# Kernel optimization log

Hardware: AMD Instinct MI355X
Metric: run time of the kernel (lower is better)

The kernel has to match this reference:

```python
import jax, jax.numpy as jnp
import numpy as np

JACCARD_THRESH = 0.5
NEGPOS_RATIO = 3
V0, V1 = 0.1, 0.2  # SSD encoding variances


def setup_inputs() -> dict:
    key = jax.random.key(0)
    k1, k2, k3, k4, k5, k6, k7 = jax.random.split(key, 7)
    B, P, C, O = 128, 8732, 21, 16
    loc_data = jax.random.normal(k1, (B, P, 4), dtype=jnp.float32)
    conf_data = jax.random.normal(k2, (B, P, C), dtype=jnp.float32)
    # default boxes in center form (cx, cy, w, h), all in [0,1]
    cxcy = jax.random.uniform(k3, (P, 2), minval=0.05, maxval=0.95)
    wh = jax.random.uniform(k4, (P, 2), minval=0.05, maxval=0.6)
    dbox_list = jnp.concatenate([cxcy, wh], axis=1).astype(jnp.float32)
    # ground-truth boxes in corner form with guaranteed positive extent
    tl = jax.random.uniform(k5, (B, O, 2), minval=0.0, maxval=0.6)
    sz = jax.random.uniform(k6, (B, O, 2), minval=0.05, maxval=0.35)
    labels = jax.random.randint(k7, (B, O, 1), 0, C - 1).astype(jnp.float32)
    targets = jnp.concatenate([tl, tl + sz, labels], axis=2)
    return {"loc_data": loc_data, "conf_data": conf_data,
            "dbox_list": dbox_list, "targets": targets}


def _match_one(truths, labels, dbox):
    """SSD match for one image. truths:[O,4] corner, labels:[O], dbox:[P,4] center."""
    pf = jnp.concatenate([dbox[:, :2] - dbox[:, 2:] * 0.5,
                          dbox[:, :2] + dbox[:, 2:] * 0.5], axis=1)  # point form [P,4]
    lt = jnp.maximum(truths[:, None, :2], pf[None, :, :2])
    rb = jnp.minimum(truths[:, None, 2:], pf[None, :, 2:])
    whi = jnp.clip(rb - lt, 0.0)
    inter = whi[..., 0] * whi[..., 1]                                # [O,P]
    area_t = (truths[:, 2] - truths[:, 0]) * (truths[:, 3] - truths[:, 1])
    area_p = dbox[:, 2] * dbox[:, 3]
    ov = inter / (area_t[:, None] + area_p[None, :] - inter)         # jaccard [O,P]
    best_prior_idx = jnp.argmax(ov, axis=1)                          # [O]
    bto = jnp.max(ov, axis=0)                                        # [P]
    bti = jnp.argmax(ov, axis=0)                                     # [P]
    bto = bto.at[best_prior_idx].set(2.0)
    O = truths.shape[0]
    bti = jax.lax.fori_loop(0, O, lambda j, b: b.at[best_prior_idx[j]].set(j), bti)
    matched = truths[bti]                                            # [P,4]
    conf = labels[bti].astype(jnp.int32) + 1
    conf = jnp.where(bto < JACCARD_THRESH, 0, conf)
    g_cxcy = ((matched[:, :2] + matched[:, 2:]) * 0.5 - dbox[:, :2]) / (V0 * dbox[:, 2:])
    g_wh = jnp.log((matched[:, 2:] - matched[:, :2]) / dbox[:, 2:]) / V1
    return jnp.concatenate([g_cxcy, g_wh], axis=1), conf


def reference(loc_data, conf_data, dbox_list, targets):
    B, P, C = conf_data.shape
    loc_t, conf_t = jax.vmap(_match_one, in_axes=(0, 0, None))(
        targets[..., :4], targets[..., 4], dbox_list)
    pos = conf_t > 0                                                  # [B,P]
    # smooth L1 (beta=1), summed over positives
    ad = jnp.abs(loc_data - loc_t)
    sl1 = jnp.where(ad < 1.0, 0.5 * ad * ad, ad - 0.5)
    loss_l = jnp.sum(jnp.where(pos[..., None], sl1, 0.0))
    # per-prior cross entropy
    logp = jax.nn.log_softmax(conf_data, axis=-1)
    ce = -jnp.take_along_axis(logp, conf_t[..., None], axis=-1)[..., 0]  # [B,P]
    # hard negative mining via double argsort (rank in descending order)
    ce_neg = jnp.where(pos, 0.0, ce)
    loss_idx = jnp.argsort(-ce_neg, axis=1)
    idx_rank = jnp.argsort(loss_idx, axis=1)
    num_pos = jnp.sum(pos, axis=1, keepdims=True)
    num_neg = jnp.minimum(num_pos * NEGPOS_RATIO, P)
    neg = idx_rank < num_neg
    sel = pos | neg
    loss_c = jnp.sum(jnp.where(sel, ce, 0.0))
    N = jnp.sum(num_pos).astype(loc_data.dtype)
    return jnp.stack([loss_l / N, loss_c / N])
```

## Files before the change

### kernel.cpp

```cpp
#include <hip/hip_runtime.h>
#include <cstddef>

#define Bn 128
#define Pn 8732
#define Cn 21
#define On 16
#define MAGIC 0x13579BDFu

__device__ __forceinline__ void argmax_combine(float& v, int& p, float v2, int p2) {
  if (v2 > v || (v2 == v && p2 < p)) { v = v2; p = p2; }
}

__global__ __launch_bounds__(256) void stream_kernel(
    const float* __restrict__ conf, const float* __restrict__ dbox,
    const float* __restrict__ targets,
    float* __restrict__ ce0, unsigned char* __restrict__ pack,
    unsigned long long* __restrict__ keys) {
  const int wb = threadIdx.x >> 6, lane = threadIdx.x & 63;
  const int wave_g = blockIdx.x * 4 + wb;
  const int b = wave_g & 127;
  const int cg = wave_g >> 7;

  __shared__ float4 s_row4[4][336];
  __shared__ float s_tt[4][On * 5];
  __shared__ float s_ar[4][On];

  #pragma unroll
  for (int i = lane; i < On * 5; i += 64)
    s_tt[wb][i] = targets[(size_t)b * On * 5 + i];
  if (lane < On) {
    float x1 = targets[(size_t)b * On * 5 + lane * 5 + 0];
    float y1 = targets[(size_t)b * On * 5 + lane * 5 + 1];
    float x2 = targets[(size_t)b * On * 5 + lane * 5 + 2];
    float y2 = targets[(size_t)b * On * 5 + lane * 5 + 3];
    s_ar[wb][lane] = (x2 - x1) * (y2 - y1);
  }

  float bestv[On]; int bestp[On];
  #pragma unroll
  for (int j = 0; j < On; j++) { bestv[j] = -1.0f; bestp[j] = 0x7fffffff; }

  #pragma unroll
  for (int i = 0; i < 3; i++) {
    const int ci = cg + 64 * i;
    if (ci >= 137) break;
    const int p0 = ci * 64;
    const int rows = min(64, Pn - p0);
    const int n4 = rows * Cn / 4;

    const float4* src = (const float4*)(conf + ((size_t)b * Pn + p0) * Cn);
    float4 v0, v1, v2, v3, v4, v5;
    if (lane < n4)        v0 = src[lane];
    if (lane + 64 < n4)   v1 = src[lane + 64];
    if (lane + 128 < n4)  v2 = src[lane + 128];
    if (lane + 192 < n4)  v3 = src[lane + 192];
    if (lane + 256 < n4)  v4 = src[lane + 256];
    if (lane + 320 < n4)  v5 = src[lane + 320];
    if (lane < n4)        s_row4[wb][lane] = v0;
    if (lane + 64 < n4)   s_row4[wb][lane + 64] = v1;
    if (lane + 128 < n4)  s_row4[wb][lane + 128] = v2;
    if (lane + 192 < n4)  s_row4[wb][lane + 192] = v3;
    if (lane + 256 < n4)  s_row4[wb][lane + 256] = v4;
    if (lane + 320 < n4)  s_row4[wb][lane + 320] = v5;

    if (lane < rows) {
      const int p = p0 + lane;
      const float* x = (const float*)s_row4[wb] + lane * Cn;
      float m = x[0];
      #pragma unroll
      for (int q = 1; q < Cn; q++) m = fmaxf(m, x[q]);
      float s = 0.0f;
      #pragma unroll
      for (int q = 0; q < Cn; q++) s += __expf(x[q] - m);
      float lse = m + __logf(s);
      ce0[(size_t)b * Pn + p] = lse - x[0];

      float4 d = ((const float4*)dbox)[p];
      float px1 = d.x - d.z * 0.5f, py1 = d.y - d.w * 0.5f;
      float px2 = d.x + d.z * 0.5f, py2 = d.y + d.w * 0.5f;
      float ap = d.z * d.w;
      float mv = -1.0f; int mj = 0;
      #pragma unroll
      for (int j = 0; j < On; j++) {
        float lx = fmaxf(s_tt[wb][j*5+0], px1);
        float ly = fmaxf(s_tt[wb][j*5+1], py1);
        float rx = fminf(s_tt[wb][j*5+2], px2);
        float ry = fminf(s_tt[wb][j*5+3], py2);
        float w = fmaxf(rx - lx, 0.0f), h = fmaxf(ry - ly, 0.0f);
        float inter = w * h;
        float ov = __fdividef(inter, s_ar[wb][j] + ap - inter);
        if (ov > bestv[j]) { bestv[j] = ov; bestp[j] = p; }
        if (ov > mv) { mv = ov; mj = j; }
      }
      pack[(size_t)b * Pn + p] =
          (unsigned char)(mj | ((mv >= 0.5f) ? 16 : 0));
    }
  }

  #pragma unroll
  for (int j = 0; j < On; j++) {
    float v = bestv[j]; int p = bestp[j];
    #pragma unroll
    for (int off = 32; off; off >>= 1) {
      float v2 = __shfl_down(v, off);
      int p2 = __shfl_down(p, off);
      argmax_combine(v, p, v2, p2);
    }
    if (lane == 0) {
      unsigned long long key;
      if (v < 0.0f) key = 0xC000000000000000ull;
      else key = (((unsigned long long)(__float_as_uint(v) | 0xC0000000u)) << 32)
               | (unsigned long long)(0xFFFFFFFFu - (unsigned)p);
      atomicMax(&keys[b * On + j], key);
    }
  }
}

__global__ __launch_bounds__(1024) void reduce_kernel(
    const float* __restrict__ loc, const float* __restrict__ conf,
    const float* __restrict__ dbox, const float* __restrict__ targets,
    const float* __restrict__ ce0, const unsigned char* __restrict__ pack,
    const unsigned long long* __restrict__ keys,
    unsigned int* __restrict__ res, float* __restrict__ out) {
  const int b = blockIdx.x;
  const int tid = threadIdx.x;
  const int wave = tid >> 6, lane = tid & 63;

  __shared__ float s_t[On * 5];
  __shared__ int s_bp[On];
  __shared__ unsigned hist[256 * 16];
  __shared__ unsigned s_col[256];
  __shared__ unsigned s_cand[64];
  __shared__ float s_redf[2][16];
  __shared__ int s_redi[16];
  __shared__ unsigned s_prefix;
  __shared__ int s_kk;
  __shared__ int s_cnt;
  __shared__ int s_cc;
  __shared__ int s_np;

  if (tid < On * 5) s_t[tid] = targets[(size_t)b * On * 5 + tid];
  if (tid < On)
    s_bp[tid] = (int)(0xFFFFFFFFu - (unsigned)(keys[b * On + tid] & 0xFFFFFFFFull));
  __syncthreads();

  float ce_r[9];
  float my_loc = 0.0f, my_cep = 0.0f; int my_np = 0;
  #pragma unroll
  for (int sI = 0; sI < 9; sI++) {
    ce_r[sI] = 0.0f;
    const int p = tid + 1024 * sI;
    if (p < Pn) {
      unsigned char pk = pack[(size_t)b * Pn + p];
      float c0 = ce0[(size_t)b * Pn + p];
      int pos = pk >> 4;
      int bt = pk & 15;
      #pragma unroll
      for (int j = 0; j < On; j++)
        if (s_bp[j] == p) { bt = j; pos = 1; }
      ce_r[sI] = pos ? 0.0f : c0;
      if (pos) {
        my_np++;
        const float* t = &s_t[bt * 5];
        int c = (int)t[4] + 1;
        const float* row = conf + ((size_t)b * Pn + p) * Cn;
        my_cep += c0 + row[0] - row[c];
        float4 d = ((const float4*)dbox)[p];
        float mx1 = t[0], my1 = t[1], mx2 = t[2], my2 = t[3];
        float g0 = ((mx1 + mx2) * 0.5f - d.x) / (0.1f * d.z);
        float g1 = ((my1 + my2) * 0.5f - d.y) / (0.1f * d.w);
        float g2 = logf((mx2 - mx1) / d.z) / 0.2f;
        float g3 = logf((my2 - my1) / d.w) / 0.2f;
        float4 ld = ((const float4*)loc)[(size_t)b * Pn + p];
        float g[4] = {g0, g1, g2, g3};
        float l[4] = {ld.x, ld.y, ld.z, ld.w};
        #pragma unroll
        for (int q = 0; q < 4; q++) {
          float ad = fabsf(l[q] - g[q]);
          my_loc += (ad < 1.0f) ? 0.5f * ad * ad : ad - 0.5f;
        }
      }
    }
  }

  {
    int np = my_np;
    #pragma unroll
    for (int off = 32; off; off >>= 1) np += __shfl_down(np, off);
    if (lane == 0) s_redi[wave] = np;
  }
  __syncthreads();
  if (tid == 0) {
    int np = 0;
    #pragma unroll
    for (int w = 0; w < 16; w++) np += s_redi[w];
    s_np = np;
  }
  __syncthreads();

  const int k = min(s_np * 3, Pn);
  unsigned prefix = 0, maskb = 0;
  int kk = k;
  int cntc = Pn;
  for (int shift = 24; shift >= 0; shift -= 8) {
    if (cntc <= 64) break;
    ((uint4*)hist)[tid] = make_uint4(0u, 0u, 0u, 0u);
    __syncthreads();
    #pragma unroll
    for (int sI = 0; sI < 9; sI++) {
      const int p = tid + 1024 * sI;
      if (p < Pn) {
        unsigned u = __float_as_uint(ce_r[sI]);
        if ((u & maskb) == prefix)
          atomicAdd(&hist[(((u >> shift) & 255u) << 4) + (unsigned)wave], 1u);
      }
    }
    __syncthreads();
    if (tid < 256) {
      unsigned c = 0;
      #pragma unroll
      for (int w = 0; w < 16; w++) c += hist[(tid << 4) + w];
      s_col[tid] = c;
    }
    __syncthreads();
    if (tid < 64) {
      unsigned c0 = s_col[4 * tid + 0], c1 = s_col[4 * tid + 1];
      unsigned c2 = s_col[4 * tid + 2], c3 = s_col[4 * tid + 3];
      unsigned t0 = c0 + c1 + c2 + c3;
      unsigned S = t0;
      #pragma unroll
      for (int off = 1; off < 64; off <<= 1) {
        unsigned o = __shfl_down(S, off);
        if (tid + off < 64) S += o;
      }
      unsigned Snext = S - t0;
      unsigned s3 = Snext + c3;
      unsigned s2 = s3 + c2;
      unsigned s1 = s2 + c1;
      unsigned s0 = s1 + c0;
      unsigned kk_u = (unsigned)kk;
      int chosen = -1; unsigned snx = 0, cc = 0;
      if (s3 >= kk_u && Snext < kk_u)      { chosen = 3; snx = Snext; cc = c3; }
      else if (s2 >= kk_u && s3 < kk_u)    { chosen = 2; snx = s3;    cc = c2; }
      else if (s1 >= kk_u && s2 < kk_u)    { chosen = 1; snx = s2;    cc = c1; }
      else if (s0 >= kk_u && s1 < kk_u)    { chosen = 0; snx = s1;    cc = c0; }
      if (chosen >= 0) {
        s_prefix = prefix | ((unsigned)(4 * tid + chosen) << shift);
        s_kk = (int)(kk_u - snx);
        s_cnt = (int)cc;
      }
    }
    __syncthreads();
    prefix = s_prefix; kk = s_kk; cntc = s_cnt;
    maskb |= 255u << shift;
  }
  if (maskb != 0xFFFFFFFFu) {
    if (tid == 0) s_cc = 0;
    __syncthreads();
    #pragma unroll
    for (int sI = 0; sI < 9; sI++) {
      const int p = tid + 1024 * sI;
      if (p < Pn) {
        unsigned u = __float_as_uint(ce_r[sI]);
        if ((u & maskb) == prefix) {
          int ix = atomicAdd(&s_cc, 1);
          s_cand[ix] = u;
        }
      }
    }
    __syncthreads();
    if (tid < 64) {
      int c = s_cc;
      if (tid < c) {
        unsigned v = s_cand[tid];
        int g = 0, e = 0;
        for (int i = 0; i < c; i++) {
          unsigned w = s_cand[i];
          g += (w > v); e += (w == v);
        }
        if (g < kk && kk <= g + e) s_prefix = v;
      }
    }
    __syncthreads();
    prefix = s_prefix;
  }
  float T = __uint_as_float(prefix);

  float sum_gt = 0.0f; int cnt_gt = 0;
  #pragma unroll
  for (int sI = 0; sI < 9; sI++) {
    const int p = tid + 1024 * sI;
    if (p < Pn) {
      float x = ce_r[sI];
      if (x > T) { sum_gt += x; cnt_gt++; }
    }
  }
  #pragma unroll
  for (int off = 32; off; off >>= 1) {
    sum_gt += __shfl_down(sum_gt, off);
    cnt_gt += __shfl_down(cnt_gt, off);
    my_loc += __shfl_down(my_loc, off);
    my_cep += __shfl_down(my_cep, off);
  }
  if (lane == 0) {
    s_redf[0][wave] = my_loc; s_redf[1][wave] = sum_gt + my_cep; s_redi[wave] = cnt_gt;
  }
  __syncthreads();
  if (tid == 0) {
    float ll = 0.0f, lc = 0.0f; int cg = 0;
    #pragma unroll
    for (int w = 0; w < 16; w++) {
      ll += s_redf[0][w]; lc += s_redf[1][w]; cg += s_redi[w];
    }
    lc += (k > 0) ? (float)(k - cg) * T : 0.0f;
    atomicExch(&res[b * 4 + 0], __float_as_uint(ll));
    atomicExch(&res[b * 4 + 1], __float_as_uint(lc));
    atomicExch(&res[b * 4 + 2], (unsigned)s_np);
    __threadfence();
    atomicExch(&res[b * 4 + 3], MAGIC);
  }

  if (b == 0 && tid < 64) {
    float ll = 0.0f, lc = 0.0f; int np = 0;
    #pragma unroll
    for (int h = 0; h < 2; h++) {
      const int i = tid + 64 * h;
      while (atomicAdd(&res[i * 4 + 3], 0u) != MAGIC) { __builtin_amdgcn_s_sleep(8); }
      ll += __uint_as_float(atomicAdd(&res[i * 4 + 0], 0u));
      lc += __uint_as_float(atomicAdd(&res[i * 4 + 1], 0u));
      np += (int)atomicAdd(&res[i * 4 + 2], 0u);
    }
    #pragma unroll
    for (int off = 32; off; off >>= 1) {
      ll += __shfl_down(ll, off);
      lc += __shfl_down(lc, off);
      np += __shfl_down(np, off);
    }
    if (tid == 0) {
      float fN = (float)np;
      out[0] = ll / fN;
      out[1] = lc / fN;
    }
  }
}

extern "C" void kernel_launch(void* const* d_in, const int* in_sizes, int n_in,
                              void* d_out, int out_size, void* d_ws, size_t ws_size,
                              hipStream_t stream) {
  const float* loc_data  = (const float*)d_in[0];
  const float* conf_data = (const float*)d_in[1];
  const float* dbox      = (const float*)d_in[2];
  const float* targets   = (const float*)d_in[3];
  float* out = (float*)d_out;

  char* ws = (char*)d_ws;
  float* ce0 = (float*)ws;
  unsigned char* pack = (unsigned char*)(ws + (size_t)Bn * Pn * 4);
  unsigned long long* keys =
      (unsigned long long*)(ws + (size_t)Bn * Pn * 5);
  unsigned int* res = (unsigned int*)(ws + (size_t)Bn * Pn * 5 + Bn * On * 8);

  stream_kernel<<<2048, 256, 0, stream>>>(conf_data, dbox, targets, ce0, pack, keys);
  reduce_kernel<<<Bn, 1024, 0, stream>>>(loc_data, conf_data, dbox, targets,
                                         ce0, pack, keys, res, out);
}
```

Measured before the change: 205.2 us.

## Halve stream grid and handle forced-match priors via bitmask and dedicated wave

The stream kernel now launches half as many blocks, and each wave walks up to five 64-prior chunks instead of three. In the reduce kernel, the 16-way compare per prior is replaced by a shared bitmask lookup of the forced best-prior indices. Those forced priors have their CE and localization loss computed separately by wave 0 with a full log-sum-exp, presumably because ce0 may not hold the right value for them. It also uses the fast __logf intrinsic and bounds the candidate buffer writes, trading a little accuracy and some added serial work in wave 0 for less per-prior overhead.

```diff
diff --git a/kernel.cpp b/kernel.cpp
--- a/kernel.cpp
+++ b/kernel.cpp
@@ -9,6 +9,20 @@
 
 __device__ __forceinline__ void argmax_combine(float& v, int& p, float v2, int p2) {
   if (v2 > v || (v2 == v && p2 < p)) { v = v2; p = p2; }
+}
+
+__device__ __forceinline__ float sl1_enc(float4 lv, float4 d,
+                                         float t0, float t1, float t2, float t3) {
+  float g0 = ((t0 + t2) * 0.5f - d.x) / (0.1f * d.z);
+  float g1 = ((t1 + t3) * 0.5f - d.y) / (0.1f * d.w);
+  float g2 = __logf((t2 - t0) / d.z) / 0.2f;
+  float g3 = __logf((t3 - t1) / d.w) / 0.2f;
+  float r = 0.f, a;
+  a = fabsf(lv.x - g0); r += (a < 1.f) ? 0.5f * a * a : a - 0.5f;
+  a = fabsf(lv.y - g1); r += (a < 1.f) ? 0.5f * a * a : a - 0.5f;
+  a = fabsf(lv.z - g2); r += (a < 1.f) ? 0.5f * a * a : a - 0.5f;
+  a = fabsf(lv.w - g3); r += (a < 1.f) ? 0.5f * a * a : a - 0.5f;
+  return r;
 }
 
 __global__ __launch_bounds__(256) void stream_kernel(
@@ -25,7 +39,6 @@
   __shared__ float s_tt[4][On * 5];
   __shared__ float s_ar[4][On];
 
-  #pragma unroll
   for (int i = lane; i < On * 5; i += 64)
     s_tt[wb][i] = targets[(size_t)b * On * 5 + i];
   if (lane < On) {
@@ -41,8 +54,8 @@
   for (int j = 0; j < On; j++) { bestv[j] = -1.0f; bestp[j] = 0x7fffffff; }
 
   #pragma unroll
-  for (int i = 0; i < 3; i++) {
-    const int ci = cg + 64 * i;
+  for (int i = 0; i < 5; i++) {
+    const int ci = cg + 32 * i;
     if (ci >= 137) break;
     const int p0 = ci * 64;
     const int rows = min(64, Pn - p0);
@@ -128,6 +141,7 @@
 
   __shared__ float s_t[On * 5];
   __shared__ int s_bp[On];
+  __shared__ unsigned s_bm[273];
   __shared__ unsigned hist[256 * 16];
   __shared__ unsigned s_col[256];
   __shared__ unsigned s_cand[64];
@@ -138,11 +152,48 @@
   __shared__ int s_cnt;
   __shared__ int s_cc;
   __shared__ int s_np;
+  __shared__ float s_floc, s_fcep;
 
   if (tid < On * 5) s_t[tid] = targets[(size_t)b * On * 5 + tid];
-  if (tid < On)
-    s_bp[tid] = (int)(0xFFFFFFFFu - (unsigned)(keys[b * On + tid] & 0xFFFFFFFFull));
+  if (tid < 273) s_bm[tid] = 0;
   __syncthreads();
+  if (tid < On) {
+    int bp = (int)(0xFFFFFFFFu - (unsigned)(keys[b * On + tid] & 0xFFFFFFFFull));
+    s_bp[tid] = bp;
+    atomicOr(&s_bm[bp >> 5], 1u << (bp & 31));
+  }
+  __syncthreads();
+
+  if (wave == 0) {
+    float f_loc = 0.f, f_cep = 0.f;
+    const bool valid = lane < On;
+    const int p = valid ? s_bp[lane] : 0;
+    bool dup = false;
+    if (valid)
+      for (int j2 = lane + 1; j2 < On; j2++) dup |= (s_bp[j2] == p);
+    if (valid && !dup) {
+      const float* row = conf + ((size_t)b * Pn + p) * Cn;
+      float m = row[0];
+      #pragma unroll
+      for (int q = 1; q < Cn; q++) m = fmaxf(m, row[q]);
+      float s = 0.f;
+      #pragma unroll
+      for (int q = 0; q < Cn; q++) s += __expf(row[q] - m);
+      const float lse = m + __logf(s);
+      const int c = (int)s_t[lane * 5 + 4] + 1;
+      f_cep = lse - row[c];
+      const float4 d = ((const float4*)dbox)[p];
+      const float4 lv = ((const float4*)loc)[(size_t)b * Pn + p];
+      f_loc = sl1_enc(lv, d, s_t[lane*5+0], s_t[lane*5+1],
+                             s_t[lane*5+2], s_t[lane*5+3]);
+    }
+    #pragma unroll
+    for (int off = 32; off; off >>= 1) {
+      f_loc += __shfl_down(f_loc, off);
+      f_cep += __shfl_down(f_cep, off);
+    }
+    if (lane == 0) { s_floc = f_loc; s_fcep = f_cep; }
+  }
 
   float ce_r[9];
   float my_loc = 0.0f, my_cep = 0.0f; int my_np = 0;
@@ -153,32 +204,20 @@
     if (p < Pn) {
       unsigned char pk = pack[(size_t)b * Pn + p];
       float c0 = ce0[(size_t)b * Pn + p];
-      int pos = pk >> 4;
-      int bt = pk & 15;
-      #pragma unroll
-      for (int j = 0; j < On; j++)
-        if (s_bp[j] == p) { bt = j; pos = 1; }
+      const unsigned forced = (s_bm[p >> 5] >> (p & 31)) & 1u;
+      const int posb = (pk >> 4);
+      const int pos = posb | (int)forced;
       ce_r[sI] = pos ? 0.0f : c0;
-      if (pos) {
-        my_np++;
+      if (pos) my_np++;
+      if (posb && !forced) {
+        const int bt = pk & 15;
         const float* t = &s_t[bt * 5];
         int c = (int)t[4] + 1;
         const float* row = conf + ((size_t)b * Pn + p) * Cn;
         my_cep += c0 + row[0] - row[c];
         float4 d = ((const float4*)dbox)[p];
-        float mx1 = t[0], my1 = t[1], mx2 = t[2], my2 = t[3];
-        float g0 = ((mx1 + mx2) * 0.5f - d.x) / (0.1f * d.z);
-        float g1 = ((my1 + my2) * 0.5f - d.y) / (0.1f * d.w);
-        float g2 = logf((mx2 - mx1) / d.z) / 0.2f;
-        float g3 = logf((my2 - my1) / d.w) / 0.2f;
         float4 ld = ((const float4*)loc)[(size_t)b * Pn + p];
-        float g[4] = {g0, g1, g2, g3};
-        float l[4] = {ld.x, ld.y, ld.z, ld.w};
-        #pragma unroll
-        for (int q = 0; q < 4; q++) {
-          float ad = fabsf(l[q] - g[q]);
-          my_loc += (ad < 1.0f) ? 0.5f * ad * ad : ad - 0.5f;
-        }
+        my_loc += sl1_enc(ld, d, t[0], t[1], t[2], t[3]);
       }
     }
   }
@@ -264,13 +303,13 @@
         unsigned u = __float_as_uint(ce_r[sI]);
         if ((u & maskb) == prefix) {
           int ix = atomicAdd(&s_cc, 1);
-          s_cand[ix] = u;
+          if (ix < 64) s_cand[ix] = u;
         }
       }
     }
     __syncthreads();
     if (tid < 64) {
-      int c = s_cc;
+      int c = min(s_cc, 64);
       if (tid < c) {
         unsigned v = s_cand[tid];
         int g = 0, e = 0;
@@ -307,12 +346,12 @@
   }
   __syncthreads();
   if (tid == 0) {
-    float ll = 0.0f, lc = 0.0f; int cg = 0;
+    float ll = s_floc, lc = s_fcep; int cg2 = 0;
     #pragma unroll
     for (int w = 0; w < 16; w++) {
-      ll += s_redf[0][w]; lc += s_redf[1][w]; cg += s_redi[w];
-    }
-    lc += (k > 0) ? (float)(k - cg) * T : 0.0f;
+      ll += s_redf[0][w]; lc += s_redf[1][w]; cg2 += s_redi[w];
+    }
+    lc += (k > 0) ? (float)(k - cg2) * T : 0.0f;
     atomicExch(&res[b * 4 + 0], __float_as_uint(ll));
     atomicExch(&res[b * 4 + 1], __float_as_uint(lc));
     atomicExch(&res[b * 4 + 2], (unsigned)s_np);
@@ -360,7 +399,7 @@
       (unsigned long long*)(ws + (size_t)Bn * Pn * 5);
   unsigned int* res = (unsigned int*)(ws + (size_t)Bn * Pn * 5 + Bn * On * 8);
 
-  stream_kernel<<<2048, 256, 0, stream>>>(conf_data, dbox, targets, ce0, pack, keys);
+  stream_kernel<<<1024, 256, 0, stream>>>(conf_data, dbox, targets, ce0, pack, keys);
   reduce_kernel<<<Bn, 1024, 0, stream>>>(loc_data, conf_data, dbox, targets,
                                          ce0, pack, keys, res, out);
 }
```

New measurement: 202.3 us. No clear change (-1.4%).
